# Kernel tuning notes

Hardware: AMD Instinct MI355X
Metric: run time of the kernel (lower is better)

## Reference

```python
import jax, jax.numpy as jnp
import numpy as np

B = 16384          # batch size
NUM_NEG = 4
N = 1 + NUM_NEG    # items per row (pos + negs)
D = 128            # embedding_dim
F = 4              # num_factors
FS = D // F        # factor_size = 32
TD = 384           # bert_text_dim
NU = 100000        # num_users
NI = 100000        # num_items
HID = 150          # text MLP hidden
M = 2              # num_modalities


def _linear_init(k, fan_out, fan_in):
    bound = 1.0 / np.sqrt(fan_in)
    return jax.random.uniform(k, (fan_out, fan_in), jnp.float32, -bound, bound)


def setup_inputs() -> dict:
    key = jax.random.key(0)
    ks = jax.random.split(key, 12)
    batch = jax.random.randint(ks[0], (B, 1 + N), 0, NU)          # col0=user, cols1..5=items
    text = jax.random.normal(ks[1], (B, N, TD), dtype=jnp.float32)
    user_table = jax.random.normal(ks[2], (NU, D), dtype=jnp.float32)
    item_table = jax.random.normal(ks[3], (NI, D), dtype=jnp.float32)
    w1 = _linear_init(ks[4], HID, TD)
    b1 = jax.random.uniform(ks[5], (HID,), jnp.float32, -1/np.sqrt(TD), 1/np.sqrt(TD))
    w2 = _linear_init(ks[6], D, HID)
    b2 = jax.random.uniform(ks[7], (D,), jnp.float32, -1/np.sqrt(HID), 1/np.sqrt(HID))
    # per-factor attention MLPs, stacked over the F factors (all same size here)
    aw1 = jax.random.uniform(ks[8], (F, M, 3 * FS), jnp.float32, -1/np.sqrt(3*FS), 1/np.sqrt(3*FS))
    ab1 = jax.random.uniform(ks[9], (F, M), jnp.float32, -1/np.sqrt(3*FS), 1/np.sqrt(3*FS))
    aw2 = jax.random.uniform(ks[10], (F, M, M), jnp.float32, -1/np.sqrt(M), 1/np.sqrt(M))
    return dict(batch=batch, text=text, user_table=user_table, item_table=item_table,
                w1=w1, b1=b1, w2=w2, b2=b2, aw1=aw1, ab1=ab1, aw2=aw2)


def _leaky_relu(x):
    return jnp.where(x > 0, x, 0.01 * x)


def reference(batch, text, user_table, item_table, w1, b1, w2, b2, aw1, ab1, aw2):
    # text MLP: Linear -> LeakyReLU -> Linear -> LeakyReLU
    te = _leaky_relu(_leaky_relu(text @ w1.T + b1) @ w2.T + b2)   # [B,N,D]

    users = batch[:, 0]
    items = batch[:, 1:]
    u = user_table[users]                                          # [B,D]
    ie = item_table[items]                                         # [B,N,D]

    # split into F factors of size FS (vectorized over factor dim)
    uf = jnp.broadcast_to(u[:, None, :], ie.shape).reshape(B, N, F, FS)
    itf = ie.reshape(B, N, F, FS)
    tf = te.reshape(B, N, F, FS)

    cat = jnp.concatenate([uf, itf, tf], axis=-1)                  # [B,N,F,3*FS]
    nrm = jnp.linalg.norm(cat, axis=-1, keepdims=True)
    cat = cat / jnp.maximum(nrm, 1e-12)                            # F.normalize(dim=-1)

    h = jnp.tanh(jnp.einsum('bnfk,fmk->bnfm', cat, aw1) + ab1)     # [B,N,F,M]
    logits = jnp.einsum('bnfm,fom->bnfo', h, aw2)                  # [B,N,F,M]
    # torch nn.Softmax() with dim=None on a 3D tensor -> softmax over dim 0 (batch)
    attn = jax.nn.softmax(logits, axis=0)

    r_ui = attn[..., 0] * jax.nn.softplus(jnp.sum(uf * itf, axis=-1))  # [B,N,F]
    r_ut = attn[..., 1] * jax.nn.softplus(jnp.sum(uf * tf, axis=-1))   # [B,N,F]
    ratings = jnp.sum(r_ui + r_ut, axis=-1)                        # [B,N], sum over factors
    return ratings
```

## Files before the change

### kernel.cpp

```cpp
#include <hip/hip_runtime.h>
#include <hip/hip_bf16.h>

#define TDIM 384
#define HID 150
#define DD 128
#define ROWS 81920
#define RT 64

typedef __attribute__((ext_vector_type(8))) short short8;
typedef __attribute__((ext_vector_type(4))) float f32x4;

#define AS_OFF   0
#define WS1_OFF  5120
#define HS_OFF   0
#define WS2_OFF  21504
#define SMEM_BYTES 31744

__device__ __forceinline__ float lrelu(float x) { return x > 0.f ? x : 0.01f * x; }
__device__ __forceinline__ float softplusf(float x) {
    return fmaxf(x, 0.f) + log1pf(expf(-fabsf(x)));
}

__device__ __forceinline__ short8 pack8(const float4 a, const float4 b) {
    union { short8 s; __hip_bfloat16 h[8]; } u;
    u.h[0] = __float2bfloat16(a.x); u.h[1] = __float2bfloat16(a.y);
    u.h[2] = __float2bfloat16(a.z); u.h[3] = __float2bfloat16(a.w);
    u.h[4] = __float2bfloat16(b.x); u.h[5] = __float2bfloat16(b.y);
    u.h[6] = __float2bfloat16(b.z); u.h[7] = __float2bfloat16(b.w);
    return u.s;
}

__global__ __launch_bounds__(256, 5)
void gemm_te(const float* __restrict__ text,
             const float* __restrict__ w1,
             const float* __restrict__ b1,
             const float* __restrict__ w2,
             const float* __restrict__ b2,
             float* __restrict__ te)
{
    __shared__ __align__(16) unsigned char smem[SMEM_BYTES];
    __hip_bfloat16* As  = (__hip_bfloat16*)(smem + AS_OFF);
    __hip_bfloat16* Ws1 = (__hip_bfloat16*)(smem + WS1_OFF);
    __hip_bfloat16* Hs  = (__hip_bfloat16*)(smem + HS_OFF);
    __hip_bfloat16* Ws2 = (__hip_bfloat16*)(smem + WS2_OFF);

    const int t    = threadIdx.x;
    const int r0   = blockIdx.x * RT;
    const int lane = t & 63;
    const int wv   = t >> 6;
    const int m16  = lane & 15;
    const int quad = lane >> 4;
    const int wr   = (wv & 1) * 32;
    const int wc   = (wv >> 1) * 80;
    const int wc2  = (wv >> 1) * 64;

    const int srow = t >> 2;
    const int sko  = (t & 3) * 8;
    const bool hasx = (t < 128);

    f32x4 acc1[2][5];
#pragma unroll
    for (int i = 0; i < 2; ++i)
#pragma unroll
        for (int j = 0; j < 5; ++j) acc1[i][j] = (f32x4){0.f, 0.f, 0.f, 0.f};

    float4 pa0, pa1;
    float4 pw[3][2];

    auto loadA = [&](int kt) {
        const float* p = &text[(size_t)(r0 + srow) * TDIM + kt * 32 + sko];
        pa0 = *(const float4*)p;
        pa1 = *(const float4*)(p + 4);
    };
    auto loadW1 = [&](int kt) {
#pragma unroll
        for (int h = 0; h < 3; ++h) {
            if (h == 2 && !hasx) continue;
            const int row = srow + 64 * h;
            if (row < HID) {
                const float* p = &w1[(size_t)row * TDIM + kt * 32 + sko];
                pw[h][0] = *(const float4*)p;
                pw[h][1] = *(const float4*)(p + 4);
            } else {
                pw[h][0] = make_float4(0.f, 0.f, 0.f, 0.f);
                pw[h][1] = make_float4(0.f, 0.f, 0.f, 0.f);
            }
        }
    };

    loadA(0);
    loadW1(0);
    for (int kt = 0; kt < 12; ++kt) {
        *(short8*)&As[srow * 40 + sko] = pack8(pa0, pa1);
#pragma unroll
        for (int h = 0; h < 3; ++h) {
            if (h == 2 && !hasx) continue;
            const int row = srow + 64 * h;
            *(short8*)&Ws1[row * 40 + sko] = pack8(pw[h][0], pw[h][1]);
        }
        __syncthreads();
        if (kt < 11) { loadA(kt + 1); loadW1(kt + 1); }

        const short8 a0 = *(const short8*)&As[(wr + m16) * 40 + quad * 8];
        const short8 a1 = *(const short8*)&As[(wr + 16 + m16) * 40 + quad * 8];
#pragma unroll
        for (int tj = 0; tj < 5; ++tj) {
            const short8 b = *(const short8*)&Ws1[(wc + tj * 16 + m16) * 40 + quad * 8];
            acc1[0][tj] = __builtin_amdgcn_mfma_f32_16x16x32_bf16(a0, b, acc1[0][tj], 0, 0, 0);
            acc1[1][tj] = __builtin_amdgcn_mfma_f32_16x16x32_bf16(a1, b, acc1[1][tj], 0, 0, 0);
        }
        __syncthreads();
    }

    float pw2[2][8];
    auto loadW2 = [&](int kt) {
        const int k0 = kt * 32;
#pragma unroll
        for (int h = 0; h < 2; ++h) {
            const int row = srow + 64 * h + ((t >> 31) & 0);
            (void)row;
        }
#pragma unroll
        for (int h = 0; h < 2; ++h) {
            const int idx = t + h * 256;
            const int row = idx >> 2;
            const int ko  = (idx & 3) * 8;
            const int k   = k0 + ko;
#pragma unroll
            for (int j = 0; j < 8; ++j)
                pw2[h][j] = (k + j < HID) ? w2[(size_t)row * HID + k + j] : 0.f;
        }
    };
    auto storeW2 = [&]() {
#pragma unroll
        for (int h = 0; h < 2; ++h) {
            const int idx = t + h * 256;
            const int row = idx >> 2;
            const int ko  = (idx & 3) * 8;
            union { short8 s; __hip_bfloat16 hb[8]; } u;
#pragma unroll
            for (int j = 0; j < 8; ++j) u.hb[j] = __float2bfloat16(pw2[h][j]);
            *(short8*)&Ws2[row * 40 + ko] = u.s;
        }
    };

    loadW2(0);

#pragma unroll
    for (int tj = 0; tj < 5; ++tj) {
        const int col = wc + tj * 16 + m16;
        const float bv = (col < HID) ? b1[col] : 0.f;
#pragma unroll
        for (int ti = 0; ti < 2; ++ti) {
#pragma unroll
            for (int r = 0; r < 4; ++r) {
                const int row = wr + ti * 16 + quad * 4 + r;
                float v = lrelu(acc1[ti][tj][r] + bv);
                if (col >= HID) v = 0.f;
                Hs[row * 168 + col] = __float2bfloat16(v);
            }
        }
    }
    storeW2();
    __syncthreads();

    f32x4 acc2[2][4];
#pragma unroll
    for (int i = 0; i < 2; ++i)
#pragma unroll
        for (int j = 0; j < 4; ++j) acc2[i][j] = (f32x4){0.f, 0.f, 0.f, 0.f};

#pragma unroll
    for (int kt = 0; kt < 5; ++kt) {
        if (kt < 4) loadW2(kt + 1);
        const int k0 = kt * 32;
        const short8 a0 = *(const short8*)&Hs[(wr + m16) * 168 + k0 + quad * 8];
        const short8 a1 = *(const short8*)&Hs[(wr + 16 + m16) * 168 + k0 + quad * 8];
#pragma unroll
        for (int tj = 0; tj < 4; ++tj) {
            const short8 b = *(const short8*)&Ws2[(wc2 + tj * 16 + m16) * 40 + quad * 8];
            acc2[0][tj] = __builtin_amdgcn_mfma_f32_16x16x32_bf16(a0, b, acc2[0][tj], 0, 0, 0);
            acc2[1][tj] = __builtin_amdgcn_mfma_f32_16x16x32_bf16(a1, b, acc2[1][tj], 0, 0, 0);
        }
        __syncthreads();
        if (kt < 4) { storeW2(); __syncthreads(); }
    }

#pragma unroll
    for (int tj = 0; tj < 4; ++tj) {
        const int col = wc2 + tj * 16 + m16;
        const float bv = b2[col];
#pragma unroll
        for (int ti = 0; ti < 2; ++ti) {
#pragma unroll
            for (int r = 0; r < 4; ++r) {
                const int row = wr + ti * 16 + quad * 4 + r;
                te[(size_t)(r0 + row) * DD + col] = lrelu(acc2[ti][tj][r] + bv);
            }
        }
    }
}

__global__ __launch_bounds__(256, 4)
void phase3(const int* __restrict__ batch,
            const float* __restrict__ user_table,
            const float* __restrict__ item_table,
            const float* __restrict__ te,
            const float* __restrict__ aw1,
            const float* __restrict__ ab1,
            const float* __restrict__ aw2,
            float* __restrict__ expp,
            float* __restrict__ Sglob)
{
    __shared__ float S_lds[40];
    const int t = threadIdx.x;
    if (t < 40) S_lds[t] = 0.f;
    __syncthreads();

    const int row = t >> 2;
    const int f   = t & 3;
    const int gr  = blockIdx.x * 64 + row;
    const int b   = gr / 5;
    const int n   = gr - b * 5;
    const int uid = batch[b * 6];
    const int iid = batch[b * 6 + 1 + n];
    const float* up  = user_table + (size_t)uid * DD + f * 32;
    const float* ip  = item_table + (size_t)iid * DD + f * 32;
    const float* tp  = te + (size_t)gr * DD + f * 32;
    const float* a1p = aw1 + f * 2 * 96;

    float ss = 0.f, z0 = 0.f, z1 = 0.f, sui = 0.f, sut = 0.f;
#pragma unroll
    for (int q = 0; q < 8; ++q) {
        const float4 u4 = *(const float4*)(up + q * 4);
        const float4 e4 = *(const float4*)(ip + q * 4);
        const float4 t4 = *(const float4*)(tp + q * 4);
        const float uu[4] = {u4.x, u4.y, u4.z, u4.w};
        const float ee[4] = {e4.x, e4.y, e4.z, e4.w};
        const float tt[4] = {t4.x, t4.y, t4.z, t4.w};
#pragma unroll
        for (int c = 0; c < 4; ++c) {
            const int i = q * 4 + c;
            const float u = uu[c], e = ee[c], x = tt[c];
            ss  = fmaf(u, u, ss); ss = fmaf(e, e, ss); ss = fmaf(x, x, ss);
            z0  = fmaf(u, a1p[i],       z0);
            z0  = fmaf(e, a1p[32 + i],  z0);
            z0  = fmaf(x, a1p[64 + i],  z0);
            z1  = fmaf(u, a1p[96 + i],  z1);
            z1  = fmaf(e, a1p[128 + i], z1);
            z1  = fmaf(x, a1p[160 + i], z1);
            sui = fmaf(u, e, sui);
            sut = fmaf(u, x, sut);
        }
    }
    const float inv = 1.f / fmaxf(sqrtf(ss), 1e-12f);
    const float h0 = tanhf(fmaf(z0, inv, ab1[f * 2 + 0]));
    const float h1 = tanhf(fmaf(z1, inv, ab1[f * 2 + 1]));
    const float l0 = fmaf(h0, aw2[f * 4 + 0], h1 * aw2[f * 4 + 1]);
    const float l1 = fmaf(h0, aw2[f * 4 + 2], h1 * aw2[f * 4 + 3]);
    const float e0 = expf(l0), e1 = expf(l1);
    const float pui = softplusf(sui), put = softplusf(sut);
    *(float4*)&expp[((size_t)gr * 4 + f) * 4] = make_float4(e0, e1, pui, put);
    atomicAdd(&S_lds[n * 8 + f * 2 + 0], e0);
    atomicAdd(&S_lds[n * 8 + f * 2 + 1], e1);
    __syncthreads();
    if (t < 40) atomicAdd(&Sglob[t * 32], S_lds[t]);
}

__global__ void finalize(const float* __restrict__ expp,
                         const float* __restrict__ Sglob,
                         float* __restrict__ out)
{
    const int gr = blockIdx.x * 256 + threadIdx.x;
    if (gr >= ROWS) return;
    const int b = gr / 5;
    const int n = gr - b * 5;
    float r = 0.f;
#pragma unroll
    for (int f = 0; f < 4; ++f) {
        const float4 v = *(const float4*)&expp[((size_t)gr * 4 + f) * 4];
        const float S0 = Sglob[(n * 8 + f * 2 + 0) * 32];
        const float S1 = Sglob[(n * 8 + f * 2 + 1) * 32];
        r += v.x / S0 * v.z + v.y / S1 * v.w;
    }
    out[gr] = r;
}

extern "C" void kernel_launch(void* const* d_in, const int* in_sizes, int n_in,
                              void* d_out, int out_size, void* d_ws, size_t ws_size,
                              hipStream_t stream)
{
    (void)in_sizes; (void)n_in; (void)out_size; (void)ws_size;
    const int*   batch      = (const int*)d_in[0];
    const float* text       = (const float*)d_in[1];
    const float* user_table = (const float*)d_in[2];
    const float* item_table = (const float*)d_in[3];
    const float* w1         = (const float*)d_in[4];
    const float* b1         = (const float*)d_in[5];
    const float* w2         = (const float*)d_in[6];
    const float* b2         = (const float*)d_in[7];
    const float* aw1        = (const float*)d_in[8];
    const float* ab1        = (const float*)d_in[9];
    const float* aw2        = (const float*)d_in[10];
    float* out = (float*)d_out;

    float* te    = (float*)d_ws;
    float* expp  = te + (size_t)ROWS * DD;
    float* Sglob = expp + (size_t)ROWS * 16;

    hipMemsetAsync(Sglob, 0, 40 * 32 * sizeof(float), stream);
    gemm_te<<<ROWS / RT, 256, 0, stream>>>(text, w1, b1, w2, b2, te);
    phase3<<<ROWS / 64, 256, 0, stream>>>(batch, user_table, item_table, te,
                                          aw1, ab1, aw2, expp, Sglob);
    finalize<<<(ROWS + 255) / 256, 256, 0, stream>>>(expp, Sglob, out);
}
```

Measured before the change: 369.9 us.

## Fuse text MLP and attention phase into one kernel with double-buffered LDS

Merges the text-MLP GEMM kernel and the per-factor attention kernel into a single kernel, so the text embeddings stay in LDS instead of round-tripping through global memory. It also double-buffers the A/W1 and W2 LDS tiles, which removes one barrier per K step, and prefetches the user/item embedding rows ahead of the second GEMM to hide gather latency. The cost is a larger LDS footprint and more live registers, so the occupancy hint drops from 5 to 3 blocks per CU.

Measured after the change: 356.5 us. 3.6% less time.

```diff
diff --git a/kernel.cpp b/kernel.cpp
--- a/kernel.cpp
+++ b/kernel.cpp
@@ -10,11 +10,7 @@
 typedef __attribute__((ext_vector_type(8))) short short8;
 typedef __attribute__((ext_vector_type(4))) float f32x4;
 
-#define AS_OFF   0
-#define WS1_OFF  5120
-#define HS_OFF   0
-#define WS2_OFF  21504
-#define SMEM_BYTES 31744
+#define SMEM_BYTES 41984
 
 __device__ __forceinline__ float lrelu(float x) { return x > 0.f ? x : 0.01f * x; }
 __device__ __forceinline__ float softplusf(float x) {
@@ -30,19 +26,25 @@
     return u.s;
 }
 
-__global__ __launch_bounds__(256, 5)
-void gemm_te(const float* __restrict__ text,
-             const float* __restrict__ w1,
-             const float* __restrict__ b1,
-             const float* __restrict__ w2,
-             const float* __restrict__ b2,
-             float* __restrict__ te)
+__global__ __launch_bounds__(256, 3)
+void fused_main(const int* __restrict__ batch,
+                const float* __restrict__ text,
+                const float* __restrict__ user_table,
+                const float* __restrict__ item_table,
+                const float* __restrict__ w1,
+                const float* __restrict__ b1,
+                const float* __restrict__ w2,
+                const float* __restrict__ b2,
+                const float* __restrict__ aw1,
+                const float* __restrict__ ab1,
+                const float* __restrict__ aw2,
+                float* __restrict__ expp,
+                float* __restrict__ Sglob)
 {
     __shared__ __align__(16) unsigned char smem[SMEM_BYTES];
-    __hip_bfloat16* As  = (__hip_bfloat16*)(smem + AS_OFF);
-    __hip_bfloat16* Ws1 = (__hip_bfloat16*)(smem + WS1_OFF);
-    __hip_bfloat16* Hs  = (__hip_bfloat16*)(smem + HS_OFF);
-    __hip_bfloat16* Ws2 = (__hip_bfloat16*)(smem + WS2_OFF);
+    __shared__ float S_lds[40];
+    __hip_bfloat16* Hs = (__hip_bfloat16*)(smem);
+    float*          Ts = (float*)(smem);
 
     const int t    = threadIdx.x;
     const int r0   = blockIdx.x * RT;
@@ -57,6 +59,16 @@
     const int srow = t >> 2;
     const int sko  = (t & 3) * 8;
     const bool hasx = (t < 128);
+
+    const int p3row = t >> 2;
+    const int p3f   = t & 3;
+    const int gr    = r0 + p3row;
+    const int bb    = gr / 5;
+    const int nn    = gr - bb * 5;
+    const int uid   = batch[bb * 6];
+    const int iid   = batch[bb * 6 + 1 + nn];
+
+    if (t < 40) S_lds[t] = 0.f;
 
     f32x4 acc1[2][5];
 #pragma unroll
@@ -87,20 +99,25 @@
             }
         }
     };
-
-    loadA(0);
-    loadW1(0);
-    for (int kt = 0; kt < 12; ++kt) {
+    auto store1 = [&](int p) {
+        __hip_bfloat16* As  = (__hip_bfloat16*)(smem + p * 5120);
+        __hip_bfloat16* Ws1 = (__hip_bfloat16*)(smem + 10240 + p * 12800);
         *(short8*)&As[srow * 40 + sko] = pack8(pa0, pa1);
 #pragma unroll
         for (int h = 0; h < 3; ++h) {
             if (h == 2 && !hasx) continue;
-            const int row = srow + 64 * h;
-            *(short8*)&Ws1[row * 40 + sko] = pack8(pw[h][0], pw[h][1]);
-        }
-        __syncthreads();
+            *(short8*)&Ws1[(srow + 64 * h) * 40 + sko] = pack8(pw[h][0], pw[h][1]);
+        }
+    };
+
+    loadA(0); loadW1(0);
+    store1(0);
+    __syncthreads();
+    for (int kt = 0; kt < 12; ++kt) {
         if (kt < 11) { loadA(kt + 1); loadW1(kt + 1); }
-
+        const int p = kt & 1;
+        const __hip_bfloat16* As  = (const __hip_bfloat16*)(smem + p * 5120);
+        const __hip_bfloat16* Ws1 = (const __hip_bfloat16*)(smem + 10240 + p * 12800);
         const short8 a0 = *(const short8*)&As[(wr + m16) * 40 + quad * 8];
         const short8 a1 = *(const short8*)&As[(wr + 16 + m16) * 40 + quad * 8];
 #pragma unroll
@@ -109,17 +126,13 @@
             acc1[0][tj] = __builtin_amdgcn_mfma_f32_16x16x32_bf16(a0, b, acc1[0][tj], 0, 0, 0);
             acc1[1][tj] = __builtin_amdgcn_mfma_f32_16x16x32_bf16(a1, b, acc1[1][tj], 0, 0, 0);
         }
+        if (kt < 11) store1((kt + 1) & 1);
         __syncthreads();
     }
 
     float pw2[2][8];
     auto loadW2 = [&](int kt) {
         const int k0 = kt * 32;
-#pragma unroll
-        for (int h = 0; h < 2; ++h) {
-            const int row = srow + 64 * h + ((t >> 31) & 0);
-            (void)row;
-        }
 #pragma unroll
         for (int h = 0; h < 2; ++h) {
             const int idx = t + h * 256;
@@ -131,7 +144,8 @@
                 pw2[h][j] = (k + j < HID) ? w2[(size_t)row * HID + k + j] : 0.f;
         }
     };
-    auto storeW2 = [&]() {
+    auto store2 = [&](int p) {
+        __hip_bfloat16* Ws2 = (__hip_bfloat16*)(smem + 21504 + p * 10240);
 #pragma unroll
         for (int h = 0; h < 2; ++h) {
             const int idx = t + h * 256;
@@ -161,8 +175,17 @@
             }
         }
     }
-    storeW2();
+    store2(0);
     __syncthreads();
+
+    const float* up = user_table + (size_t)uid * DD + p3f * 32;
+    const float* ip = item_table + (size_t)iid * DD + p3f * 32;
+    float4 ur[8], er[8];
+#pragma unroll
+    for (int q = 0; q < 8; ++q) {
+        ur[q] = *(const float4*)(up + q * 4);
+        er[q] = *(const float4*)(ip + q * 4);
+    }
 
     f32x4 acc2[2][4];
 #pragma unroll
@@ -174,6 +197,7 @@
     for (int kt = 0; kt < 5; ++kt) {
         if (kt < 4) loadW2(kt + 1);
         const int k0 = kt * 32;
+        const __hip_bfloat16* Ws2 = (const __hip_bfloat16*)(smem + 21504 + (kt & 1) * 10240);
         const short8 a0 = *(const short8*)&Hs[(wr + m16) * 168 + k0 + quad * 8];
         const short8 a1 = *(const short8*)&Hs[(wr + 16 + m16) * 168 + k0 + quad * 8];
 #pragma unroll
@@ -182,8 +206,8 @@
             acc2[0][tj] = __builtin_amdgcn_mfma_f32_16x16x32_bf16(a0, b, acc2[0][tj], 0, 0, 0);
             acc2[1][tj] = __builtin_amdgcn_mfma_f32_16x16x32_bf16(a1, b, acc2[1][tj], 0, 0, 0);
         }
+        if (kt < 4) store2((kt + 1) & 1);
         __syncthreads();
-        if (kt < 4) { storeW2(); __syncthreads(); }
     }
 
 #pragma unroll
@@ -195,74 +219,62 @@
 #pragma unroll
             for (int r = 0; r < 4; ++r) {
                 const int row = wr + ti * 16 + quad * 4 + r;
-                te[(size_t)(r0 + row) * DD + col] = lrelu(acc2[ti][tj][r] + bv);
+                Ts[row * 132 + col] = lrelu(acc2[ti][tj][r] + bv);
             }
         }
     }
-}
-
-__global__ __launch_bounds__(256, 4)
-void phase3(const int* __restrict__ batch,
-            const float* __restrict__ user_table,
-            const float* __restrict__ item_table,
-            const float* __restrict__ te,
-            const float* __restrict__ aw1,
-            const float* __restrict__ ab1,
-            const float* __restrict__ aw2,
-            float* __restrict__ expp,
-            float* __restrict__ Sglob)
-{
-    __shared__ float S_lds[40];
-    const int t = threadIdx.x;
-    if (t < 40) S_lds[t] = 0.f;
     __syncthreads();
 
-    const int row = t >> 2;
-    const int f   = t & 3;
-    const int gr  = blockIdx.x * 64 + row;
-    const int b   = gr / 5;
-    const int n   = gr - b * 5;
-    const int uid = batch[b * 6];
-    const int iid = batch[b * 6 + 1 + n];
-    const float* up  = user_table + (size_t)uid * DD + f * 32;
-    const float* ip  = item_table + (size_t)iid * DD + f * 32;
-    const float* tp  = te + (size_t)gr * DD + f * 32;
-    const float* a1p = aw1 + f * 2 * 96;
-
-    float ss = 0.f, z0 = 0.f, z1 = 0.f, sui = 0.f, sut = 0.f;
-#pragma unroll
-    for (int q = 0; q < 8; ++q) {
-        const float4 u4 = *(const float4*)(up + q * 4);
-        const float4 e4 = *(const float4*)(ip + q * 4);
-        const float4 t4 = *(const float4*)(tp + q * 4);
-        const float uu[4] = {u4.x, u4.y, u4.z, u4.w};
-        const float ee[4] = {e4.x, e4.y, e4.z, e4.w};
-        const float tt[4] = {t4.x, t4.y, t4.z, t4.w};
-#pragma unroll
-        for (int c = 0; c < 4; ++c) {
-            const int i = q * 4 + c;
-            const float u = uu[c], e = ee[c], x = tt[c];
-            ss  = fmaf(u, u, ss); ss = fmaf(e, e, ss); ss = fmaf(x, x, ss);
-            z0  = fmaf(u, a1p[i],       z0);
-            z0  = fmaf(e, a1p[32 + i],  z0);
-            z0  = fmaf(x, a1p[64 + i],  z0);
-            z1  = fmaf(u, a1p[96 + i],  z1);
-            z1  = fmaf(e, a1p[128 + i], z1);
-            z1  = fmaf(x, a1p[160 + i], z1);
-            sui = fmaf(u, e, sui);
-            sut = fmaf(u, x, sut);
-        }
-    }
-    const float inv = 1.f / fmaxf(sqrtf(ss), 1e-12f);
-    const float h0 = tanhf(fmaf(z0, inv, ab1[f * 2 + 0]));
-    const float h1 = tanhf(fmaf(z1, inv, ab1[f * 2 + 1]));
-    const float l0 = fmaf(h0, aw2[f * 4 + 0], h1 * aw2[f * 4 + 1]);
-    const float l1 = fmaf(h0, aw2[f * 4 + 2], h1 * aw2[f * 4 + 3]);
-    const float e0 = expf(l0), e1 = expf(l1);
-    const float pui = softplusf(sui), put = softplusf(sut);
-    *(float4*)&expp[((size_t)gr * 4 + f) * 4] = make_float4(e0, e1, pui, put);
-    atomicAdd(&S_lds[n * 8 + f * 2 + 0], e0);
-    atomicAdd(&S_lds[n * 8 + f * 2 + 1], e1);
+    {
+        const float* tp  = Ts + p3row * 132 + p3f * 32;
+        const float* a1p = aw1 + p3f * 2 * 96;
+
+        float ss = 0.f, z0 = 0.f, z1 = 0.f, sui = 0.f, sut = 0.f;
+#pragma unroll
+        for (int q = 0; q < 8; ++q) {
+            const float4 u4 = ur[q];
+            const float4 e4 = er[q];
+            const float4 t4 = *(const float4*)(tp + q * 4);
+            const float4 a00 = *(const float4*)(a1p + q * 4);
+            const float4 a01 = *(const float4*)(a1p + 32 + q * 4);
+            const float4 a02 = *(const float4*)(a1p + 64 + q * 4);
+            const float4 a10 = *(const float4*)(a1p + 96 + q * 4);
+            const float4 a11 = *(const float4*)(a1p + 128 + q * 4);
+            const float4 a12 = *(const float4*)(a1p + 160 + q * 4);
+            const float uu[4] = {u4.x, u4.y, u4.z, u4.w};
+            const float ee[4] = {e4.x, e4.y, e4.z, e4.w};
+            const float tt[4] = {t4.x, t4.y, t4.z, t4.w};
+            const float w00[4] = {a00.x, a00.y, a00.z, a00.w};
+            const float w01[4] = {a01.x, a01.y, a01.z, a01.w};
+            const float w02[4] = {a02.x, a02.y, a02.z, a02.w};
+            const float w10[4] = {a10.x, a10.y, a10.z, a10.w};
+            const float w11[4] = {a11.x, a11.y, a11.z, a11.w};
+            const float w12[4] = {a12.x, a12.y, a12.z, a12.w};
+#pragma unroll
+            for (int c = 0; c < 4; ++c) {
+                const float u = uu[c], e = ee[c], x = tt[c];
+                ss  = fmaf(u, u, ss); ss = fmaf(e, e, ss); ss = fmaf(x, x, ss);
+                z0  = fmaf(u, w00[c], z0);
+                z0  = fmaf(e, w01[c], z0);
+                z0  = fmaf(x, w02[c], z0);
+                z1  = fmaf(u, w10[c], z1);
+                z1  = fmaf(e, w11[c], z1);
+                z1  = fmaf(x, w12[c], z1);
+                sui = fmaf(u, e, sui);
+                sut = fmaf(u, x, sut);
+            }
+        }
+        const float inv = 1.f / fmaxf(sqrtf(ss), 1e-12f);
+        const float h0 = tanhf(fmaf(z0, inv, ab1[p3f * 2 + 0]));
+        const float h1 = tanhf(fmaf(z1, inv, ab1[p3f * 2 + 1]));
+        const float l0 = fmaf(h0, aw2[p3f * 4 + 0], h1 * aw2[p3f * 4 + 1]);
+        const float l1 = fmaf(h0, aw2[p3f * 4 + 2], h1 * aw2[p3f * 4 + 3]);
+        const float e0 = expf(l0), e1 = expf(l1);
+        const float pui = softplusf(sui), put = softplusf(sut);
+        *(float4*)&expp[((size_t)gr * 4 + p3f) * 4] = make_float4(e0, e1, pui, put);
+        atomicAdd(&S_lds[nn * 8 + p3f * 2 + 0], e0);
+        atomicAdd(&S_lds[nn * 8 + p3f * 2 + 1], e1);
+    }
     __syncthreads();
     if (t < 40) atomicAdd(&Sglob[t * 32], S_lds[t]);
 }
@@ -304,13 +316,12 @@
     const float* aw2        = (const float*)d_in[10];
     float* out = (float*)d_out;
 
-    float* te    = (float*)d_ws;
-    float* expp  = te + (size_t)ROWS * DD;
+    float* expp  = (float*)d_ws;
     float* Sglob = expp + (size_t)ROWS * 16;
 
     hipMemsetAsync(Sglob, 0, 40 * 32 * sizeof(float), stream);
-    gemm_te<<<ROWS / RT, 256, 0, stream>>>(text, w1, b1, w2, b2, te);
-    phase3<<<ROWS / 64, 256, 0, stream>>>(batch, user_table, item_table, te,
-                                          aw1, ab1, aw2, expp, Sglob);
+    fused_main<<<ROWS / RT, 256, 0, stream>>>(batch, text, user_table, item_table,
+                                              w1, b1, w2, b2, aw1, ab1, aw2,
+                                              expp, Sglob);
     finalize<<<(ROWS + 255) / 256, 256, 0, stream>>>(expp, Sglob, out);
 }
```
